# Kernel tuning notes

Measured on AMD Instinct MI355X. Metric: run time of the kernel, lower is better.

Reference implementation:

```python
import jax, jax.numpy as jnp
import numpy as np

NUM_BFS_ROUNDS = 32      # fixed-iteration replacement for the set-based BFS (enough hops for N=4096, k=20)
VORONOI_CHUNK = 1024     # must divide B*N


def _knn_self(points, K):
    # brute-force self-KNN over [B,N,3]; idx[...,0] is the query point itself
    sq = jnp.sum(points * points, -1)
    dist = sq[:, :, None] + sq[:, None, :] - 2.0 * jnp.einsum('bnd,bmd->bnm', points, points)
    N = points.shape[1]
    dist = jnp.where(jnp.eye(N, dtype=bool)[None], -1.0, dist)  # force self to rank first
    _, idx = jax.lax.top_k(-dist, K)
    return idx  # [B,N,K] int32


def _gather(x, idx):
    # x [B,N,D], idx [B,N,K] -> [B,N,K,D]
    return jax.vmap(lambda xb, ib: xb[ib])(x, idx)


def _disambiguate(normals, idx):
    # BFS normal-orientation propagation from point 0 (frontier shared across batch, as in the torch code)
    B, N, _ = normals.shape
    frontier0 = jnp.zeros((N,), bool).at[0].set(True)
    visited0 = jnp.zeros((N,), bool)

    def step(carry, _):
        nrm, visited, frontier = carry
        safe_idx = jnp.where(frontier[None, :, None], idx, N)  # non-frontier rows scatter to dummy slot N
        cur = _gather(nrm, idx)                                 # [B,N,K,3]
        sign = jnp.where(jnp.sum(cur * cur[:, :, 0:1, :], -1, keepdims=True) > 0, 1.0, -1.0)
        renew = cur * sign

        def scat(nb, ib, rb):
            pad = jnp.concatenate([nb, jnp.zeros((1, 3), nb.dtype)], 0)
            return pad.at[ib.reshape(-1)].set(rb.reshape(-1, 3))[:N]

        nrm = jax.vmap(scat)(nrm, safe_idx, renew)
        mark = jnp.zeros((N + 1,), bool).at[safe_idx[:, :, 1:].reshape(-1)].set(True)[:N]
        visited = visited | frontier
        frontier = mark & ~visited
        return (nrm, visited, frontier), None

    (normals, _, _), _ = jax.lax.scan(step, (normals, visited0, frontier0), None, length=NUM_BFS_ROUNDS)
    return normals


def _frames_field(points, idx):
    knn_pts = _gather(points, idx)                              # [B,N,K,3]
    centered = knn_pts - knn_pts.mean(-2, keepdims=True)
    # NOTE: divides by (last_dim - 1) == 2, faithfully replicating the original code
    cov = jnp.einsum('bnki,bnkj->bnij', centered, centered) / 2.0
    _, vecs = jnp.linalg.eigh(cov)                              # ascending eigenvalues
    frames = jnp.swapaxes(vecs, -1, -2)                         # rows = eigenvectors; row 0 = normal
    frames = frames.at[:, :, 0, :].set(_disambiguate(frames[:, :, 0, :], idx))
    det = jnp.linalg.det(frames)
    frames = frames.at[:, :, 1, :].set(frames[:, :, 1, :] * det[..., None])
    return frames, knn_pts


def _forward(points, k, local_W):
    B, N = points.shape[:2]
    idx = _knn_self(points, k)
    frames, knn_pts = _frames_field(points, idx)
    dpt = knn_pts - points[:, :, None, :]                       # [B,N,K,3]
    t1 = frames[:, :, 1, :]
    t2 = frames[:, :, 2, :]
    dpt_t = jnp.stack([jnp.sum(dpt * t1[:, :, None, :], -1),
                       jnp.sum(dpt * t2[:, :, None, :], -1)], -1)   # [B,N,K,2]

    # ---- local voronoi area on tangent-plane grid ----
    bmin = dpt_t.min(-2) * 1.1                                  # [B,N,2]
    bmax = dpt_t.max(-2) * 1.1
    maxlen = (bmax - bmin).max(-1)                              # [B,N]
    coord = (dpt_t - bmin[:, :, None, :]) / maxlen[:, :, None, None] * 2.0 - 1.0
    lin = jnp.linspace(-1.0, 1.0, local_W, dtype=points.dtype)
    X, Y = jnp.meshgrid(lin, lin, indexing='ij')
    grid = jnp.stack([X, Y], -1).reshape(-1, 2)                 # [W^2, 2]
    coords_c = jax.lax.stop_gradient(coord).reshape(-1, VORONOI_CHUNK, k, 2)

    def chunk_count(c):  # c [C,k,2] -> count of grid cells whose nearest local point is the center (idx 0)
        d = jnp.sum((grid[None, :, None, :] - c[:, None, :, :]) ** 2, -1)  # [C,W^2,k]
        return jnp.sum(jnp.argmin(d, -1) == 0, -1)

    counts = jax.lax.map(chunk_count, coords_c).reshape(B, N).astype(points.dtype)
    area = counts * maxlen ** 2 / float((local_W - 1) ** 2)     # [B,N]

    # ---- Weingarten fields (non-strict branch) -> gaussian curvature ----
    normals = frames[:, :, 0, :]
    dnrm = _gather(normals, idx) - normals[:, :, None, :]
    dnrm_t = jnp.stack([jnp.sum(dnrm * t1[:, :, None, :], -1),
                        jnp.sum(dnrm * t2[:, :, None, :], -1)], -1)  # [B,N,K,2]
    XXT = jnp.einsum('bnki,bnkj->bnij', dpt_t, dpt_t)
    YXT = jnp.einsum('bnki,bnkj->bnij', dnrm_t, dpt_t)
    Wmat = YXT @ jnp.linalg.inv(XXT + 1e-8 * jnp.eye(2, dtype=points.dtype))
    Wmat = (Wmat + jnp.swapaxes(Wmat, -1, -2)) / 2.0
    gauss = jnp.linalg.det(Wmat)                                # [B,N]

    euler = jnp.sum(gauss * area, -1) / np.pi / 2.0             # [B]
    return euler


def setup_inputs() -> dict:
    key = jax.random.key(0)
    pointscloud = jax.random.normal(key, (2, 4096, 3), dtype=jnp.float32)
    return {"pointscloud": pointscloud, "k": 20, "local_W": 64}


def reference(pointscloud, k, local_W):
    return _forward(pointscloud, k, local_W)
```

## Files before the change

kernel.cpp:

```cpp
#include <hip/hip_runtime.h>
#include <math.h>

#define NPTS  4096
#define BATCH 2
#define KNB   20
#define WGRID 64
#define GCELLS (WGRID * WGRID)
#define NROUNDS 32
#define KBUF  192
#define KQ    8
#define NEDGE (BATCH * NPTS * KNB)
#define NPACK (NEDGE / 16)

__global__ __launch_bounds__(256) void prep_kernel(const float* __restrict__ pts,
                                                   float4* __restrict__ pts4) {
    const int i = blockIdx.x * 256 + threadIdx.x;
    const float x = pts[i * 3 + 0], y = pts[i * 3 + 1], z = pts[i * 3 + 2];
    pts4[i] = make_float4(x, y, z, x * x + y * y + z * z);
}

__global__ __launch_bounds__(512) void knn_kernel(const float4* __restrict__ pts4,
                                                  int* __restrict__ idx) {
    const int tid  = threadIdx.x;
    const int lane = tid & 63;
    const int wid  = tid >> 6;
    const int q    = blockIdx.x * KQ + wid;
    const int b    = q >> 12;
    const int n    = q & (NPTS - 1);
    const float4* P4 = pts4 + (size_t)b * NPTS;

    __shared__ float4 spts[NPTS];
    __shared__ unsigned long long buf[KQ][KBUF];

    for (int i = tid; i < NPTS; i += 512) spts[i] = P4[i];
    __syncthreads();

    const float4 me = spts[n];
    const float px = me.x, py = me.y, pz = me.z, sqn = me.w;

    float d[64];
    float lmin = 3e38f;
#pragma unroll
    for (int step = 0; step < 64; ++step) {
        const int m = lane + step * 64;
        const float4 c = spts[m];
        const float dot = px * c.x + py * c.y + pz * c.z;
        float dist = (sqn + c.w) - 2.0f * dot;
        if (m == n) dist = -1.0f;
        d[step] = dist;
        lmin = fminf(lmin, dist);
    }

    float v = lmin;
#pragma unroll
    for (int k = 2; k <= 64; k <<= 1) {
#pragma unroll
        for (int j = k >> 1; j >= 1; j >>= 1) {
            const float o = __shfl_xor(v, j, 64);
            const bool up    = ((lane & k) == 0);
            const bool lower = ((lane & j) == 0);
            v = (lower == up) ? fminf(v, o) : fmaxf(v, o);
        }
    }
    float thr = __shfl(v, 19, 64);
    thr = thr + fabsf(thr) * 1e-4f + 1e-6f;

    unsigned long long* wbuf = buf[wid];
    int cnt = 0;
#pragma unroll
    for (int step = 0; step < 64; ++step) {
        const float dist = d[step];
        const bool keep = (dist <= thr);
        const unsigned long long mask = __ballot(keep);
        if (keep) {
            const int m = lane + step * 64;
            const int pos = cnt + __popcll(mask & ((1ull << lane) - 1ull));
            unsigned u = __float_as_uint(dist);
            u = (dist < 0.0f) ? ~u : (u | 0x80000000u);
            if (pos < KBUF)
                wbuf[pos] = ((unsigned long long)u << 32) | (unsigned)m;
        }
        cnt += __popcll(mask);
    }

    const int M = (cnt < KBUF) ? cnt : KBUF;
    int* op = idx + (size_t)q * KNB;
    const unsigned long long MAXK = ~0ull;
    if (M <= 64) {
        unsigned long long key = (lane < M) ? wbuf[lane] : MAXK;
#pragma unroll
        for (int k = 2; k <= 64; k <<= 1) {
#pragma unroll
            for (int j = k >> 1; j >= 1; j >>= 1) {
                const unsigned long long o = __shfl_xor(key, j, 64);
                const bool up    = ((lane & k) == 0);
                const bool lower = ((lane & j) == 0);
                const bool takeMin = (lower == up);
                const unsigned long long mn = key < o ? key : o;
                const unsigned long long mx = key < o ? o : key;
                key = takeMin ? mn : mx;
            }
        }
        if (lane < KNB) op[lane] = (int)(unsigned)(key & 0xffffffffu);
    } else {
        unsigned long long s0 = (lane       < M) ? wbuf[lane]       : MAXK;
        unsigned long long s1 = (lane + 64  < M) ? wbuf[lane + 64]  : MAXK;
        unsigned long long s2 = (lane + 128 < M) ? wbuf[lane + 128] : MAXK;
#pragma unroll 1
        for (int r = 0; r < KNB; ++r) {
            unsigned long long kk = s0 < s1 ? s0 : s1;
            kk = kk < s2 ? kk : s2;
#pragma unroll
            for (int off = 32; off; off >>= 1) {
                const unsigned long long ok = __shfl_xor(kk, off, 64);
                kk = ok < kk ? ok : kk;
            }
            if (s0 == kk) s0 = MAXK;
            else if (s1 == kk) s1 = MAXK;
            else if (s2 == kk) s2 = MAXK;
            if (lane == 0) op[r] = (int)(unsigned)(kk & 0xffffffffu);
        }
    }
}

template <int p, int q, int r>
__device__ __forceinline__ void jrot(double A[3][3], double V[3][3]) {
    double apq = A[p][q];
    if (fabs(apq) < 1e-300) return;
    double app = A[p][p], aqq = A[q][q];
    double tau = (aqq - app) / (2.0 * apq);
    double sq  = sqrt(1.0 + tau * tau);
    double t   = (tau >= 0.0) ? (1.0 / (tau + sq)) : (1.0 / (tau - sq));
    double c   = 1.0 / sqrt(1.0 + t * t);
    double s   = t * c;
    A[p][p] = app - t * apq; A[q][q] = aqq + t * apq;
    A[p][q] = 0.0; A[q][p] = 0.0;
    double arp = A[r][p], arq = A[r][q];
    A[r][p] = c * arp - s * arq; A[p][r] = A[r][p];
    A[r][q] = s * arp + c * arq; A[q][r] = A[r][q];
#pragma unroll
    for (int i = 0; i < 3; ++i) {
        double vip = V[i][p], viq = V[i][q];
        V[i][p] = c * vip - s * viq;
        V[i][q] = s * vip + c * viq;
    }
}

__device__ __forceinline__ double selV(const double V[3][3], int i, int c) {
    return c == 0 ? V[i][0] : (c == 1 ? V[i][1] : V[i][2]);
}

__global__ __launch_bounds__(64) void frames_kernel(const float* __restrict__ pts,
                                                    const int* __restrict__ idx,
                                                    float* __restrict__ frames,
                                                    float* __restrict__ normals) {
    const int g = blockIdx.x * 64 + threadIdx.x;
    const int b = g / NPTS;
    const float* P  = pts + (size_t)b * NPTS * 3;
    const int*   ip = idx + (size_t)g * KNB;

    float mx = 0.f, my = 0.f, mz = 0.f;
#pragma unroll
    for (int k = 0; k < KNB; ++k) {
        const int j = ip[k];
        mx += P[j * 3 + 0]; my += P[j * 3 + 1]; mz += P[j * 3 + 2];
    }
    mx /= 20.0f; my /= 20.0f; mz /= 20.0f;

    float c00 = 0.f, c01 = 0.f, c02 = 0.f, c11 = 0.f, c12 = 0.f, c22 = 0.f;
#pragma unroll
    for (int k = 0; k < KNB; ++k) {
        const int j = ip[k];
        const float x = P[j * 3 + 0] - mx;
        const float y = P[j * 3 + 1] - my;
        const float z = P[j * 3 + 2] - mz;
        c00 += x * x; c01 += x * y; c02 += x * z;
        c11 += y * y; c12 += y * z; c22 += z * z;
    }
    c00 *= 0.5f; c01 *= 0.5f; c02 *= 0.5f; c11 *= 0.5f; c12 *= 0.5f; c22 *= 0.5f;

    double A[3][3] = {{c00, c01, c02}, {c01, c11, c12}, {c02, c12, c22}};
    double V[3][3] = {{1, 0, 0}, {0, 1, 0}, {0, 0, 1}};
#pragma unroll
    for (int sw = 0; sw < 10; ++sw) {
        jrot<0, 1, 2>(A, V);
        jrot<0, 2, 1>(A, V);
        jrot<1, 2, 0>(A, V);
    }
    double e0 = A[0][0], e1 = A[1][1], e2 = A[2][2];
    int o0 = 0, o1 = 1, o2 = 2;
    if (e0 > e1) { double t = e0; e0 = e1; e1 = t; int o = o0; o0 = o1; o1 = o; }
    if (e1 > e2) { double t = e1; e1 = e2; e2 = t; int o = o1; o1 = o2; o2 = o; }
    if (e0 > e1) { double t = e0; e0 = e1; e1 = t; int o = o0; o0 = o1; o1 = o; }

    float* F = frames + (size_t)g * 9;
    F[0] = (float)selV(V, 0, o0); F[1] = (float)selV(V, 1, o0); F[2] = (float)selV(V, 2, o0);
    F[3] = (float)selV(V, 0, o1); F[4] = (float)selV(V, 1, o1); F[5] = (float)selV(V, 2, o1);
    F[6] = (float)selV(V, 0, o2); F[7] = (float)selV(V, 1, o2); F[8] = (float)selV(V, 2, o2);
    normals[(size_t)g * 3 + 0] = F[0];
    normals[(size_t)g * 3 + 1] = F[1];
    normals[(size_t)g * 3 + 2] = F[2];
}

__global__ __launch_bounds__(256) void edgesign_kernel(const int* __restrict__ idx,
                                                       const float* __restrict__ normals,
                                                       unsigned* __restrict__ dsgnp,
                                                       unsigned short* __restrict__ idx16) {
    const int e = blockIdx.x * 256 + threadIdx.x;
    const int lane = threadIdx.x & 63;
    const int b = e / (NPTS * KNB);
    const int r = e - b * NPTS * KNB;
    const int n = r / KNB;
    const int j = idx[e];
    idx16[e] = (unsigned short)j;
    const float* NB = normals + (size_t)b * NPTS * 3;
    const float d = __fadd_rn(__fadd_rn(__fmul_rn(NB[j * 3 + 0], NB[n * 3 + 0]),
                                        __fmul_rn(NB[j * 3 + 1], NB[n * 3 + 1])),
                              __fmul_rn(NB[j * 3 + 2], NB[n * 3 + 2]));
    const unsigned long long m0 = __ballot(d == 0.0f);
    const unsigned long long m1 = __ballot(d > 0.0f);
    if (lane < 4) {
        unsigned x = (unsigned)(m0 >> (lane * 16)) & 0xFFFFu;
        unsigned y = (unsigned)(m1 >> (lane * 16)) & 0xFFFFu;
        x = (x | (x << 8)) & 0x00FF00FFu; x = (x | (x << 4)) & 0x0F0F0F0Fu;
        x = (x | (x << 2)) & 0x33333333u; x = (x | (x << 1)) & 0x55555555u;
        y = (y | (y << 8)) & 0x00FF00FFu; y = (y | (y << 4)) & 0x0F0F0F0Fu;
        y = (y | (y << 2)) & 0x33333333u; y = (y | (y << 1)) & 0x55555555u;
        dsgnp[((e - lane) >> 4) + lane] = x | (y << 1);
    }
}

__global__ __launch_bounds__(1024) void bfs_kernel(const unsigned short* __restrict__ idx16,
                                                   const unsigned* __restrict__ dsgnp,
                                                   float* __restrict__ nrm) {
    const int tid = threadIdx.x;
    const int lane = tid & 63;
    __shared__ int winner[BATCH * NPTS];
    __shared__ signed char sgbuf[2][BATCH * NPTS];
    __shared__ unsigned dsp[NPACK];
    __shared__ unsigned short list[NPTS];
    __shared__ unsigned char EL[NPTS];
    __shared__ int cntsh;

    for (int j = tid; j < NPTS; j += 1024) {
        winner[j] = 0; winner[NPTS + j] = 0;
        sgbuf[0][j] = 1; sgbuf[0][NPTS + j] = 1;
        EL[j] = 0;
    }
    for (int i = tid; i < NPACK; i += 1024) dsp[i] = dsgnp[i];
    if (tid == 0) { cntsh = 1; list[0] = 0; EL[0] = 1; }
    __syncthreads();

    int cur = 0;
    int rstart = 0, rend = 1;
    for (int round = 0; round < NROUNDS; ++round) {
        const int tag = (round + 1) << 17;
        const int items = (rend - rstart) * BATCH;
        for (int base = 0; base < items; base += 4096) {
            unsigned pr[4][KNB / 2];
            int tflat[4], wbase[4];
            bool ok[4];
#pragma unroll
            for (int s = 0; s < 4; ++s) {
                const int w = base + s * 1024 + tid;
                ok[s] = (w < items);
                if (ok[s]) {
                    const int i = w >> 1, b = w & 1;
                    const int n0 = (int)list[rstart + i];
                    tflat[s] = tag + n0 * KNB;
                    wbase[s] = b * NPTS;
                    const unsigned* rp =
                        (const unsigned*)(idx16 + ((size_t)b * NPTS + n0) * KNB);
#pragma unroll
                    for (int u = 0; u < KNB / 2; ++u) pr[s][u] = rp[u];
                }
            }
#pragma unroll
            for (int s = 0; s < 4; ++s) {
                if (ok[s]) {
#pragma unroll
                    for (int u = 0; u < KNB / 2; ++u) {
                        const int j0 = (int)(pr[s][u] & 0xffffu);
                        const int j1 = (int)(pr[s][u] >> 16);
                        atomicMax(&winner[wbase[s] + j0], tflat[s] + 2 * u);
                        atomicMax(&winner[wbase[s] + j1], tflat[s] + 2 * u + 1);
                    }
                }
            }
        }
        __syncthreads();
        const signed char* sgOld = sgbuf[cur];
        signed char* sgNew = sgbuf[cur ^ 1];
#pragma unroll
        for (int u = 0; u < 4; ++u) {
            const int j = tid + u * 1024;
            bool marked = false;
#pragma unroll
            for (int b = 0; b < BATCH; ++b) {
                const int bj = b * NPTS + j;
                const int w = winner[bj];
                signed char s = sgOld[bj];
                if (w >= tag) {
                    const int flat = w - tag;
                    const int nsrc = flat / KNB;
                    const int wi = b * (NPTS * KNB) + flat;
                    const int d = (int)((dsp[wi >> 4] >> ((wi & 15) << 1)) & 3u) - 1;
                    const signed char sn = sgOld[b * NPTS + nsrc];
                    s = d ? (signed char)(d * sn) : (signed char)(-s);
                    if (flat % KNB != 0) marked = true;
                }
                sgNew[bj] = s;
            }
            const bool f = marked && !EL[j];
            if (f) EL[j] = 1;
            const unsigned long long mask = __ballot(f);
            if (mask) {
                const int lead = (int)(__ffsll((long long)mask) - 1);
                int basep = 0;
                if (lane == lead) basep = atomicAdd(&cntsh, (int)__popcll(mask));
                basep = __shfl(basep, lead, 64);
                if (f) list[basep + (int)__popcll(mask & ((1ull << lane) - 1ull))] =
                           (unsigned short)j;
            }
        }
        __syncthreads();
        cur ^= 1;
        rstart = rend;
        rend = cntsh;
        if (rstart == rend) break;
    }
    const signed char* sgF = sgbuf[cur];
    for (int i = tid; i < BATCH * NPTS * 3; i += 1024) {
        if (sgF[i / 3] < 0) nrm[i] = -nrm[i];
    }
}

__global__ __launch_bounds__(256) void geom_kernel(const float* __restrict__ pts,
                                                   const int* __restrict__ idx,
                                                   const float* __restrict__ frames,
                                                   const float* __restrict__ nrm,
                                                   double* __restrict__ pervals) {
    const int lane = threadIdx.x & 63;
    const int q = blockIdx.x * 4 + (threadIdx.x >> 6);
    const int b = q >> 12, n = q & (NPTS - 1);
    const float* P  = pts + (size_t)b * NPTS * 3;
    const float* NR = nrm + (size_t)b * NPTS * 3;
    const float* F  = frames + (size_t)q * 9;

    const float v0x = NR[n * 3 + 0], v0y = NR[n * 3 + 1], v0z = NR[n * 3 + 2];
    const float v1x = F[3], v1y = F[4], v1z = F[5];
    const float v2x = F[6], v2y = F[7], v2z = F[8];
    const float det = v0x * (v1y * v2z - v1z * v2y)
                    - v0y * (v1x * v2z - v1z * v2x)
                    + v0z * (v1x * v2y - v1y * v2x);
    const float t1x = v1x * det, t1y = v1y * det, t1z = v1z * det;
    const float t2x = v2x, t2y = v2y, t2z = v2z;

    const bool isk = lane < KNB;
    float ptx = 0.f, pty = 0.f, qtx = 0.f, qty = 0.f;
    if (isk) {
        const int j = idx[(size_t)q * KNB + lane];
        const float dx = P[j * 3 + 0] - P[n * 3 + 0];
        const float dy = P[j * 3 + 1] - P[n * 3 + 1];
        const float dz = P[j * 3 + 2] - P[n * 3 + 2];
        ptx = dx * t1x + dy * t1y + dz * t1z;
        pty = dx * t2x + dy * t2y + dz * t2z;
        const float ex = NR[j * 3 + 0] - v0x;
        const float ey = NR[j * 3 + 1] - v0y;
        const float ez = NR[j * 3 + 2] - v0z;
        qtx = ex * t1x + ey * t1y + ez * t1z;
        qty = ex * t2x + ey * t2y + ez * t2z;
    }

    float mnx = isk ? ptx :  3e38f, mny = isk ? pty :  3e38f;
    float mxx = isk ? ptx : -3e38f, mxy = isk ? pty : -3e38f;
#pragma unroll
    for (int off = 32; off; off >>= 1) {
        mnx = fminf(mnx, __shfl_xor(mnx, off, 64));
        mny = fminf(mny, __shfl_xor(mny, off, 64));
        mxx = fmaxf(mxx, __shfl_xor(mxx, off, 64));
        mxy = fmaxf(mxy, __shfl_xor(mxy, off, 64));
    }
    mnx *= 1.1f; mny *= 1.1f; mxx *= 1.1f; mxy *= 1.1f;
    const float ml = fmaxf(mxx - mnx, mxy - mny);

    const float cx = (ptx - mnx) / ml * 2.0f - 1.0f;
    const float cy = (pty - mny) / ml * 2.0f - 1.0f;
    const float c0x = __shfl(cx, 0, 64), c0y = __shfl(cy, 0, 64);

    const float ax = 2.0f * (cx - c0x);
    const float ay = 2.0f * (cy - c0y);
    const float bbk = cx * cx + cy * cy - (c0x * c0x + c0y * c0y);
    const float inva = (ay != 0.0f) ? (1.0f / ay) : 0.0f;

    const float gx = (float)(-1.0 + (2.0 * (double)lane) / 63.0);
    float lo = -3e38f, hi = 3e38f;
    bool feas = true;
#pragma unroll
    for (int k = 1; k < KNB; ++k) {
        const float axk = __shfl(ax, k, 64);
        const float ayk = __shfl(ay, k, 64);
        const float bk  = __shfl(bbk, k, 64);
        const float ik  = __shfl(inva, k, 64);
        const float rk  = bk - gx * axk;
        const float t   = rk * ik;
        if (ayk > 0.0f)      hi = fminf(hi, t);
        else if (ayk < 0.0f) lo = fmaxf(lo, t);
        else                 feas = feas && (rk >= 0.0f);
    }
    int cnt = 0;
    if (feas) {
        const float hif = fminf((hi + 1.0f) * 31.5f, 63.0f);
        const float lof = fmaxf((lo + 1.0f) * 31.5f, 0.0f);
        const int jhi = (int)floorf(hif);
        const int jlo = (int)ceilf(lof);
        cnt = jhi - jlo + 1;
        if (cnt < 0) cnt = 0;
    }
#pragma unroll
    for (int off = 32; off; off >>= 1) cnt += __shfl_xor(cnt, off, 64);
    const float area = (float)cnt * ml * ml / 3969.0f;

    double xx00 = 0, xx01 = 0, xx11 = 0, yx00 = 0, yx01 = 0, yx10 = 0, yx11 = 0;
    if (isk) {
        const double px = ptx, py = pty, qx2 = qtx, qy2 = qty;
        xx00 = px * px; xx01 = px * py; xx11 = py * py;
        yx00 = qx2 * px; yx01 = qx2 * py; yx10 = qy2 * px; yx11 = qy2 * py;
    }
#pragma unroll
    for (int off = 32; off; off >>= 1) {
        xx00 += __shfl_xor(xx00, off, 64);
        xx01 += __shfl_xor(xx01, off, 64);
        xx11 += __shfl_xor(xx11, off, 64);
        yx00 += __shfl_xor(yx00, off, 64);
        yx01 += __shfl_xor(yx01, off, 64);
        yx10 += __shfl_xor(yx10, off, 64);
        yx11 += __shfl_xor(yx11, off, 64);
    }
    if (lane == 0) {
        const double m00 = xx00 + 1e-8, m01 = xx01, m11 = xx11 + 1e-8;
        const double dm = m00 * m11 - m01 * m01;
        const double i00 = m11 / dm, i01 = -m01 / dm, i11 = m00 / dm;
        const double w00 = yx00 * i00 + yx01 * i01;
        const double w01 = yx00 * i01 + yx01 * i11;
        const double w10 = yx10 * i00 + yx11 * i01;
        const double w11 = yx10 * i01 + yx11 * i11;
        const double off2 = 0.5 * (w01 + w10);
        const double gauss = w00 * w11 - off2 * off2;
        pervals[q] = gauss * (double)area;
    }
}

__global__ __launch_bounds__(256) void reduce_kernel(const double* __restrict__ pervals,
                                                     float* __restrict__ out) {
    const int b = blockIdx.x, tid = threadIdx.x;
    __shared__ double sm[256];
    double s = 0.0;
    for (int i = tid; i < NPTS; i += 256) s += pervals[(size_t)b * NPTS + i];
    sm[tid] = s;
    __syncthreads();
    for (int st = 128; st > 0; st >>= 1) {
        if (tid < st) sm[tid] += sm[tid + st];
        __syncthreads();
    }
    if (tid == 0) out[b] = (float)(sm[0] / 3.14159265358979323846 / 2.0);
}

extern "C" void kernel_launch(void* const* d_in, const int* in_sizes, int n_in,
                              void* d_out, int out_size, void* d_ws, size_t ws_size,
                              hipStream_t stream) {
    (void)in_sizes; (void)n_in; (void)out_size; (void)ws_size;
    const float* pts = (const float*)d_in[0];
    char* ws = (char*)d_ws;

    size_t off = 0;
    double* pervals = (double*)(ws + off); off += (size_t)BATCH * NPTS * sizeof(double);
    int*    idx     = (int*)(ws + off);    off += (size_t)BATCH * NPTS * KNB * sizeof(int);
    float*  frames  = (float*)(ws + off);  off += (size_t)BATCH * NPTS * 9 * sizeof(float);
    float*  normals = (float*)(ws + off);  off += (size_t)BATCH * NPTS * 3 * sizeof(float);
    unsigned short* idx16 = (unsigned short*)(ws + off);
    off += (size_t)BATCH * NPTS * KNB * sizeof(unsigned short);
    unsigned* dsgnp = (unsigned*)(ws + off);
    off += (size_t)NPACK * sizeof(unsigned);
    off = (off + 15) & ~(size_t)15;
    float4* pts4 = (float4*)(ws + off);

    prep_kernel<<<BATCH * NPTS / 256, 256, 0, stream>>>(pts, pts4);
    knn_kernel<<<BATCH * NPTS / KQ, 512, 0, stream>>>(pts4, idx);
    frames_kernel<<<BATCH * NPTS / 64, 64, 0, stream>>>(pts, idx, frames, normals);
    edgesign_kernel<<<BATCH * NPTS * KNB / 256, 256, 0, stream>>>(idx, normals, dsgnp, idx16);
    bfs_kernel<<<1, 1024, 0, stream>>>(idx16, dsgnp, normals);
    geom_kernel<<<BATCH * NPTS / 4, 256, 0, stream>>>(pts, idx, frames, normals, pervals);
    reduce_kernel<<<BATCH, 256, 0, stream>>>(pervals, (float*)d_out);
}
```

Baseline: 115.8 us.

## Recompute KNN distances instead of caching them to cut registers, double queries per block

The KNN kernel no longer keeps 64 distances per lane in registers. It recomputes them from shared memory in the threshold-compaction pass and again when building sort keys. The candidate buffer now stores 16-bit indices instead of 64-bit keys, and blocks grow to 1024 threads covering 16 queries, so each load of the point set into shared memory is shared by more queries. This trades extra ALU and LDS reads for lower register pressure and higher occupancy.

```diff
diff --git a/kernel.cpp b/kernel.cpp
--- a/kernel.cpp
+++ b/kernel.cpp
@@ -8,7 +8,7 @@
 #define GCELLS (WGRID * WGRID)
 #define NROUNDS 32
 #define KBUF  192
-#define KQ    8
+#define KQ    16
 #define NEDGE (BATCH * NPTS * KNB)
 #define NPACK (NEDGE / 16)
 
@@ -19,8 +19,24 @@
     pts4[i] = make_float4(x, y, z, x * x + y * y + z * z);
 }
 
-__global__ __launch_bounds__(512) void knn_kernel(const float4* __restrict__ pts4,
-                                                  int* __restrict__ idx) {
+__device__ __forceinline__ float knn_dist(const float4 c, const float px,
+                                          const float py, const float pz,
+                                          const float sqn, const int m,
+                                          const int n) {
+    const float dot = px * c.x + py * c.y + pz * c.z;
+    float dist = (sqn + c.w) - 2.0f * dot;
+    if (m == n) dist = -1.0f;
+    return dist;
+}
+
+__device__ __forceinline__ unsigned long long knn_key(const float dist, const int m) {
+    unsigned u = __float_as_uint(dist);
+    u = (dist < 0.0f) ? ~u : (u | 0x80000000u);
+    return ((unsigned long long)u << 32) | (unsigned)m;
+}
+
+__global__ __launch_bounds__(1024, 8) void knn_kernel(const float4* __restrict__ pts4,
+                                                      int* __restrict__ idx) {
     const int tid  = threadIdx.x;
     const int lane = tid & 63;
     const int wid  = tid >> 6;
@@ -30,25 +46,19 @@
     const float4* P4 = pts4 + (size_t)b * NPTS;
 
     __shared__ float4 spts[NPTS];
-    __shared__ unsigned long long buf[KQ][KBUF];
-
-    for (int i = tid; i < NPTS; i += 512) spts[i] = P4[i];
+    __shared__ unsigned short buf[KQ][KBUF];
+
+    for (int i = tid; i < NPTS; i += 1024) spts[i] = P4[i];
     __syncthreads();
 
     const float4 me = spts[n];
     const float px = me.x, py = me.y, pz = me.z, sqn = me.w;
 
-    float d[64];
     float lmin = 3e38f;
 #pragma unroll
     for (int step = 0; step < 64; ++step) {
         const int m = lane + step * 64;
-        const float4 c = spts[m];
-        const float dot = px * c.x + py * c.y + pz * c.z;
-        float dist = (sqn + c.w) - 2.0f * dot;
-        if (m == n) dist = -1.0f;
-        d[step] = dist;
-        lmin = fminf(lmin, dist);
+        lmin = fminf(lmin, knn_dist(spts[m], px, py, pz, sqn, m, n));
     }
 
     float v = lmin;
@@ -65,20 +75,17 @@
     float thr = __shfl(v, 19, 64);
     thr = thr + fabsf(thr) * 1e-4f + 1e-6f;
 
-    unsigned long long* wbuf = buf[wid];
+    unsigned short* wbuf = buf[wid];
     int cnt = 0;
 #pragma unroll
     for (int step = 0; step < 64; ++step) {
-        const float dist = d[step];
+        const int m = lane + step * 64;
+        const float dist = knn_dist(spts[m], px, py, pz, sqn, m, n);
         const bool keep = (dist <= thr);
         const unsigned long long mask = __ballot(keep);
         if (keep) {
-            const int m = lane + step * 64;
             const int pos = cnt + __popcll(mask & ((1ull << lane) - 1ull));
-            unsigned u = __float_as_uint(dist);
-            u = (dist < 0.0f) ? ~u : (u | 0x80000000u);
-            if (pos < KBUF)
-                wbuf[pos] = ((unsigned long long)u << 32) | (unsigned)m;
+            if (pos < KBUF) wbuf[pos] = (unsigned short)m;
         }
         cnt += __popcll(mask);
     }
@@ -87,7 +94,11 @@
     int* op = idx + (size_t)q * KNB;
     const unsigned long long MAXK = ~0ull;
     if (M <= 64) {
-        unsigned long long key = (lane < M) ? wbuf[lane] : MAXK;
+        unsigned long long key = MAXK;
+        if (lane < M) {
+            const int m = (int)wbuf[lane];
+            key = knn_key(knn_dist(spts[m], px, py, pz, sqn, m, n), m);
+        }
 #pragma unroll
         for (int k = 2; k <= 64; k <<= 1) {
 #pragma unroll
@@ -103,9 +114,19 @@
         }
         if (lane < KNB) op[lane] = (int)(unsigned)(key & 0xffffffffu);
     } else {
-        unsigned long long s0 = (lane       < M) ? wbuf[lane]       : MAXK;
-        unsigned long long s1 = (lane + 64  < M) ? wbuf[lane + 64]  : MAXK;
-        unsigned long long s2 = (lane + 128 < M) ? wbuf[lane + 128] : MAXK;
+        unsigned long long s0 = MAXK, s1 = MAXK, s2 = MAXK;
+        if (lane < M) {
+            const int m = (int)wbuf[lane];
+            s0 = knn_key(knn_dist(spts[m], px, py, pz, sqn, m, n), m);
+        }
+        if (lane + 64 < M) {
+            const int m = (int)wbuf[lane + 64];
+            s1 = knn_key(knn_dist(spts[m], px, py, pz, sqn, m, n), m);
+        }
+        if (lane + 128 < M) {
+            const int m = (int)wbuf[lane + 128];
+            s2 = knn_key(knn_dist(spts[m], px, py, pz, sqn, m, n), m);
+        }
 #pragma unroll 1
         for (int r = 0; r < KNB; ++r) {
             unsigned long long kk = s0 < s1 ? s0 : s1;
@@ -486,7 +507,7 @@
     float4* pts4 = (float4*)(ws + off);
 
     prep_kernel<<<BATCH * NPTS / 256, 256, 0, stream>>>(pts, pts4);
-    knn_kernel<<<BATCH * NPTS / KQ, 512, 0, stream>>>(pts4, idx);
+    knn_kernel<<<BATCH * NPTS / KQ, 1024, 0, stream>>>(pts4, idx);
     frames_kernel<<<BATCH * NPTS / 64, 64, 0, stream>>>(pts, idx, frames, normals);
     edgesign_kernel<<<BATCH * NPTS * KNB / 256, 256, 0, stream>>>(idx, normals, dsgnp, idx16);
     bfs_kernel<<<1, 1024, 0, stream>>>(idx16, dsgnp, normals);
```

New measurement: 105.3 us. -9.1%, faster.
